# Kernel optimization log

Hardware: AMD Instinct MI355X
Metric: run time of the kernel (lower is better)

The kernel has to match this reference:

```python
import jax, jax.numpy as jnp
import numpy as np

N = 768
SINGLE_DIM = 384
PAIR_DIM = 128
D = 16      # proj_dim per head
H = 12      # n_heads
P = 4       # n_query_points
PV = 8      # n_point_values


def _random_rotations(key, n):
    a = jax.random.normal(key, (n, 3, 3), dtype=jnp.float32)
    q, r = jnp.linalg.qr(a)
    d = jnp.sign(jnp.diagonal(r, axis1=-2, axis2=-1))
    q = q * d[:, None, :]
    det = jnp.linalg.det(q)
    return q * jnp.where(det < 0, -1.0, 1.0)[:, None, None]


def setup_inputs() -> dict:
    key = jax.random.key(0)
    ks = jax.random.split(key, 12)
    s = 0.02
    return {
        "single_rep": jax.random.normal(ks[0], (N, SINGLE_DIM), dtype=jnp.float32),
        "pair_rep": jax.random.normal(ks[1], (N, N, PAIR_DIM), dtype=jnp.float32),
        "rotations": _random_rotations(ks[2], N),
        "translations": jax.random.normal(ks[3], (N, 3), dtype=jnp.float32),
        "Wqkv": s * jax.random.normal(ks[4], (SINGLE_DIM, 3 * H * D), dtype=jnp.float32),
        "Wb": s * jax.random.normal(ks[5], (PAIR_DIM, H), dtype=jnp.float32),
        "Wqk_pts": s * jax.random.normal(ks[6], (SINGLE_DIM, 2 * H * P * 3), dtype=jnp.float32),
        "Wv_pts": s * jax.random.normal(ks[7], (SINGLE_DIM, H * PV * 3), dtype=jnp.float32),
        "gamma": 0.1 * jax.random.normal(ks[8], (H,), dtype=jnp.float32),
        "Wout": s * jax.random.normal(ks[9], (H * (PAIR_DIM + D + PV * 3 + PV), SINGLE_DIM), dtype=jnp.float32),
        "bout": jnp.zeros((SINGLE_DIM,), dtype=jnp.float32),
    }


def _apply_frames(rot, trans, pts):
    # pts: [N, P, H, 3] -> R @ pt + t per residue (dim 0)
    return jnp.einsum('nba,npha->nphb', rot, pts) + trans[:, None, None, :]


def _apply_frames_inv(rot, trans, pts):
    # R^T (pt - t)
    return jnp.einsum('nab,npha->nphb', rot, pts - trans[:, None, None, :])


def reference(single_rep, pair_rep, rotations, translations,
              Wqkv, Wb, Wqk_pts, Wv_pts, gamma, Wout, bout):
    n = single_rep.shape[0]
    sqrt_inv_dim = 1.0 / np.sqrt(D).astype(np.float32)
    w_C = np.sqrt(2.0 / (9.0 * P)).astype(np.float32)
    w_L = np.sqrt(1.0 / 3.0).astype(np.float32)

    qkv = single_rep @ Wqkv                       # [N, 3*H*D]
    q, k, v = jnp.split(qkv, 3, axis=-1)
    q = q.reshape(n, D, H)
    k = k.reshape(n, D, H)
    v = v.reshape(n, D, H)

    b = pair_rep @ Wb                             # [N, N, H]

    qk_pts = single_rep @ Wqk_pts
    q_pts, k_pts = jnp.split(qk_pts, 2, axis=-1)
    q_pts = jnp.moveaxis(q_pts.reshape(n, P, 3, H), -1, -2)   # [N, P, H, 3]
    k_pts = jnp.moveaxis(k_pts.reshape(n, P, 3, H), -1, -2)
    v_pts = jnp.moveaxis((single_rep @ Wv_pts).reshape(n, PV, 3, H), -1, -2)  # [N, PV, H, 3]

    qg = _apply_frames(rotations, translations, q_pts)  # [N, P, H, 3]
    kg = _apply_frames(rotations, translations, k_pts)

    # sum_{p,t} ||qg_i - kg_j||^2 via expansion (avoids [N,N,P,H,3])
    q_sq = jnp.sum(qg * qg, axis=(1, 3))                # [N, H]
    k_sq = jnp.sum(kg * kg, axis=(1, 3))                # [N, H]
    cross = jnp.einsum('ipht,jpht->ijh', qg, kg)        # [N, N, H]
    dist_logits = q_sq[:, None, :] + k_sq[None, :, :] - 2.0 * cross

    dp_logits = sqrt_inv_dim * jnp.einsum('idh,jdh->ijh', q, k) + b
    scale = gamma * (w_C / 2.0)                          # [H]
    a = jax.nn.softmax(w_L * (dp_logits - scale * dist_logits), axis=1)  # [N, N, H]

    out_pair = jnp.einsum('ijh,ijz->izh', a, pair_rep)   # [N, pair_dim, H]
    out_value = jnp.einsum('ijh,jdh->idh', a, v)          # [N, D, H]

    vg = _apply_frames(rotations, translations, v_pts)    # [N, PV, H, 3]
    op = jnp.einsum('ijh,jpht->ipht', a, vg)              # [N, PV, H, 3]
    out_points = _apply_frames_inv(rotations, translations, op)
    out_points_norm = jnp.linalg.norm(out_points, axis=-1)  # [N, PV, H]

    out = jnp.concatenate([
        out_pair.reshape(n, -1),
        out_value.reshape(n, -1),
        out_points.reshape(n, -1),
        out_points_norm.reshape(n, -1),
    ], axis=1)
    return out @ Wout + bout
```

## Files before the change

### kernel.cpp

```cpp
#include <hip/hip_runtime.h>
#include <math.h>

#define NN 768
#define SD 384
#define HH 12

#define W_L 0.57735026918962576f
#define W_C 0.23570226039551584f

typedef __attribute__((ext_vector_type(8))) short short8;
typedef __attribute__((ext_vector_type(4))) short short4_t;
typedef __attribute__((ext_vector_type(4))) float floatx4;
typedef unsigned short ushort_t;
typedef unsigned int uint_t;

__device__ __forceinline__ float wave_max(float v){ for(int o=32;o;o>>=1) v=fmaxf(v,__shfl_xor(v,o)); return v; }
__device__ __forceinline__ float wave_sum(float v){ for(int o=32;o;o>>=1) v+=__shfl_xor(v,o); return v; }

static __device__ __forceinline__ ushort_t f2bf(float f) {
  union { float f; uint_t u; } v; v.f = f;
  uint_t r = (v.u + 0x7FFFu + ((v.u >> 16) & 1u)) >> 16;
  return (ushort_t)r;
}
static __device__ __forceinline__ uint_t pack2bf(float lo, float hi) {
  return ((uint_t)f2bf(hi) << 16) | (uint_t)f2bf(lo);
}

__global__ __launch_bounds__(256) void k1a_gemm(
    const float* __restrict__ single, const float* __restrict__ Wqkv,
    const float* __restrict__ Wqk, const float* __restrict__ Wvp,
    float* __restrict__ raw)
{
  __shared__ float Al[64][17];
  __shared__ float Bl[16][68];
  const int tid = threadIdx.x;
  const int bm = blockIdx.x / 18, bn = blockIdx.x % 18;
  const int tr = tid >> 4, tc = tid & 15;

  const int bcol = bn*64 + (tid & 15)*4;
  const float* Wsrc; int wstride;
  if (bcol < 576)      { Wsrc = Wqkv + bcol;        wstride = 576; }
  else if (bcol < 864) { Wsrc = Wqk  + (bcol-576);  wstride = 288; }
  else                 { Wsrc = Wvp  + (bcol-864);  wstride = 288; }
  const int brow = tid >> 4;
  const int ar = tid >> 2, ac = (tid & 3)*4;

  float4 acc0 = {0,0,0,0}, acc1 = {0,0,0,0}, acc2 = {0,0,0,0}, acc3 = {0,0,0,0};

  for (int kc = 0; kc < 24; ++kc) {
    __syncthreads();
    *(float4*)&Al[ar][ac] = *(const float4*)(single + (size_t)(bm*64+ar)*SD + kc*16 + ac);
    *(float4*)&Bl[brow][(tid&15)*4] = *(const float4*)(Wsrc + (size_t)(kc*16+brow)*wstride);
    __syncthreads();
    #pragma unroll
    for (int kk = 0; kk < 16; ++kk) {
      float a0 = Al[tr*4+0][kk], a1 = Al[tr*4+1][kk], a2 = Al[tr*4+2][kk], a3 = Al[tr*4+3][kk];
      float4 bv = *(float4*)&Bl[kk][tc*4];
      acc0.x += a0*bv.x; acc0.y += a0*bv.y; acc0.z += a0*bv.z; acc0.w += a0*bv.w;
      acc1.x += a1*bv.x; acc1.y += a1*bv.y; acc1.z += a1*bv.z; acc1.w += a1*bv.w;
      acc2.x += a2*bv.x; acc2.y += a2*bv.y; acc2.z += a2*bv.z; acc2.w += a2*bv.w;
      acc3.x += a3*bv.x; acc3.y += a3*bv.y; acc3.z += a3*bv.z; acc3.w += a3*bv.w;
    }
  }
  float* o = raw + (size_t)(bm*64 + tr*4)*1152 + bn*64 + tc*4;
  *(float4*)(o)            = acc0;
  *(float4*)(o + 1152)     = acc1;
  *(float4*)(o + 2*1152)   = acc2;
  *(float4*)(o + 3*1152)   = acc3;
}

__global__ __launch_bounds__(256) void k1b_pack(
    const float* __restrict__ raw_g, const float* __restrict__ rot,
    const float* __restrict__ trans, const float* __restrict__ gamma,
    float* __restrict__ Qt, ushort_t* __restrict__ Ktb, ushort_t* __restrict__ vvT)
{
  __shared__ float raw[4][1152];
  __shared__ float gbuf[4][16][HH][3];
  const int tid = threadIdx.x;
  const int i0 = blockIdx.x * 4;

  for (int s = tid; s < 4*288; s += 256) {
    int r = s / 288, q = s % 288;
    *(float4*)(&raw[r][q*4]) = *(const float4*)(raw_g + (size_t)(i0+r)*1152 + q*4);
  }
  __syncthreads();

  for (int s = tid; s < 4*576; s += 256) {
    int r = s / 576, cc = s % 576;
    int d = (cc % 192) / HH, h = cc % HH;
    int i = i0 + r;
    float val = raw[r][cc];
    if (cc < 192)       Qt[(size_t)i*384 + h*32 + d] = 0.25f*W_L*val;
    else if (cc < 384)  Ktb[(size_t)i*384 + h*32 + d] = f2bf(val);
    else                vvT[(size_t)(h*40 + d)*768 + i] = f2bf(val);
  }
  for (int s = tid; s < 768; s += 256) {
    int r = s / 192, rem = s % 192;
    int slot = rem / HH, h = rem % HH;
    int i = i0 + r;
    int base;
    if (slot < 4) base = 576 + slot*36;
    else if (slot < 8) base = 720 + (slot-4)*36;
    else base = 864 + (slot-8)*36;
    float x0 = raw[r][base + 0*12 + h];
    float x1 = raw[r][base + 1*12 + h];
    float x2 = raw[r][base + 2*12 + h];
    const float* R = rot + (size_t)i*9;
    const float* T = trans + (size_t)i*3;
    float g0 = R[0]*x0 + R[1]*x1 + R[2]*x2 + T[0];
    float g1 = R[3]*x0 + R[4]*x1 + R[5]*x2 + T[1];
    float g2 = R[6]*x0 + R[7]*x1 + R[8]*x2 + T[2];
    gbuf[r][slot][h][0]=g0; gbuf[r][slot][h][1]=g1; gbuf[r][slot][h][2]=g2;
    if (slot < 4) {
      float sc2 = 2.0f*W_L*(gamma[h]*W_C*0.5f);
      float* q = Qt + (size_t)i*384 + h*32 + 16 + slot*3;
      q[0]=sc2*g0; q[1]=sc2*g1; q[2]=sc2*g2;
    } else if (slot < 8) {
      ushort_t* k = Ktb + (size_t)i*384 + h*32 + 16 + (slot-4)*3;
      k[0]=f2bf(g0); k[1]=f2bf(g1); k[2]=f2bf(g2);
    } else {
      ushort_t* vp = vvT + (size_t)(h*40 + 16 + (slot-8)*3)*768 + i;
      vp[0]=f2bf(g0); vp[768]=f2bf(g1); vp[2*768]=f2bf(g2);
    }
  }
  __syncthreads();
  for (int s = tid; s < 96; s += 256) {
    int r = s / 24, rem = s % 24;
    int h = rem / 2, qk = rem % 2;
    int i = i0 + r;
    float sum = 0;
    int b0 = qk ? 4 : 0;
    for (int p = 0; p < 4; ++p)
      for (int t = 0; t < 3; ++t) { float g = gbuf[r][b0+p][h][t]; sum += g*g; }
    float sc = gamma[h]*W_C*0.5f;
    if (qk == 0) {
      float* q = Qt + (size_t)i*384 + h*32;
      q[28] = -W_L*sc; q[29] = -W_L*sc*sum; q[30] = 0.f; q[31] = 0.f;
    } else {
      ushort_t* k = Ktb + (size_t)i*384 + h*32;
      k[28] = f2bf(sum); k[29] = f2bf(1.f); k[30] = 0; k[31] = 0;
    }
  }
}

__global__ __launch_bounds__(256) void k2p_logits(
    const float* __restrict__ pair, const float* __restrict__ Wb,
    const float* __restrict__ Qt, const ushort_t* __restrict__ Ktb,
    float* __restrict__ L)
{
  __shared__ ushort_t Tj[2][64*136];
  __shared__ ushort_t WbT[16*136];
  __shared__ float Qrow[384];
  const int tid = threadIdx.x;
  const int i = blockIdx.x;
  const int lane = tid & 63;
  const int w = tid >> 6;
  const int co = lane & 15, gg = lane >> 4;
  const int srow = tid >> 5, szq = tid & 31;

  for (int s = tid; s < 1536; s += 256) {
    int z = s / 12, h = s % 12;
    WbT[h*136 + z] = f2bf(W_L * Wb[s]);
  }
  for (int s = tid; s < 544; s += 256) WbT[1632 + s] = 0;
  for (int s = tid; s < 384; s += 256) Qrow[s] = Qt[(size_t)i*384 + s];

  const float* src = pair + (size_t)i*NN*128;
  float4 pr[8];
  #pragma unroll
  for (int k = 0; k < 8; ++k)
    pr[k] = *(const float4*)(src + (size_t)(srow + k*8)*128 + szq*4);

  __syncthreads();

  short8 z8, myQ, wb[4];
  #pragma unroll
  for (int s = 0; s < 8; ++s) z8[s] = 0;
  #pragma unroll
  for (int s = 0; s < 8; ++s)
    myQ[s] = (co < 12) ? (short)f2bf(Qrow[co*32 + gg*8 + s]) : (short)0;
  #pragma unroll
  for (int kt = 0; kt < 4; ++kt)
    wb[kt] = *(const short8*)&WbT[co*136 + kt*32 + gg*8];

  const int jb = w*16;

  #pragma unroll 1
  for (int t = 0; t < 12; ++t) {
    const int buf = t & 1;
    #pragma unroll
    for (int k = 0; k < 8; ++k) {
      uint2 uu;
      uu.x = pack2bf(pr[k].x, pr[k].y);
      uu.y = pack2bf(pr[k].z, pr[k].w);
      *(uint2*)&Tj[buf][(srow + k*8)*136 + szq*4] = uu;
    }
    if (t < 11) {
      const float* sn = src + (size_t)(t+1)*64*128;
      #pragma unroll
      for (int k = 0; k < 8; ++k)
        pr[k] = *(const float4*)(sn + (size_t)(srow + k*8)*128 + szq*4);
    }
    __syncthreads();

    floatx4 D; D[0]=0.f; D[1]=0.f; D[2]=0.f; D[3]=0.f;
    #pragma unroll
    for (int kt = 0; kt < 4; ++kt) {
      short8 a = *(const short8*)&Tj[buf][(jb+co)*136 + kt*32 + gg*8];
      D = __builtin_amdgcn_mfma_f32_16x16x32_bf16(a, wb[kt], D, 0, 0, 0);
    }
    const ushort_t* kr = Ktb + (size_t)(t*64 + jb + co)*384;
    #pragma unroll
    for (int kt = 0; kt < 12; ++kt) {
      short8 a = *(const short8*)(kr + kt*32 + gg*8);
      short8 b = (co == kt) ? myQ : z8;
      D = __builtin_amdgcn_mfma_f32_16x16x32_bf16(a, b, D, 0, 0, 0);
    }
    if (co < 12) {
      float4 st = {D[0], D[1], D[2], D[3]};
      *(float4*)(L + ((size_t)i*12 + co)*768 + t*64 + jb + gg*4) = st;
    }
    __syncthreads();
  }
}

__global__ __launch_bounds__(512) void k3_fused(
    const float* __restrict__ pair, const float* __restrict__ L,
    const ushort_t* __restrict__ vvT, const float* __restrict__ rot,
    const float* __restrict__ trans, float* __restrict__ C2)
{
  __shared__ ushort_t PTb[24*512];
  __shared__ ushort_t Tz[2][2][128*20];
  __shared__ float oacc[480];
  const int tid = threadIdx.x;
  const int i = (NN - 1) - blockIdx.x;
  const int w = tid >> 6, lane = tid & 63;
  const int co = lane & 15, gg = lane >> 4;

  const float* psrc = pair + (size_t)i*NN*128;
  const int f0 = tid,       pj0 = f0 >> 5, pz0 = f0 & 31;
  const int f1 = tid + 512, pj1 = f1 >> 5, pz1 = f1 & 31;

  float4 pa0, pa1, pb0, pb1;
  pa0 = *(const float4*)(psrc + (size_t)pj0*128 + pz0*4);
  pa1 = *(const float4*)(psrc + (size_t)pj1*128 + pz1*4);
  pb0 = *(const float4*)(psrc + (size_t)(32 + pj0)*128 + pz0*4);
  pb1 = *(const float4*)(psrc + (size_t)(32 + pj1)*128 + pz1*4);

  const float* Lr = L + (size_t)i*12*768;
  #pragma unroll
  for (int m = 0; m < 2; ++m) {
    if (m == 1 && w >= 4) break;
    const int h = (m == 0) ? w : 8 + w;
    const float* row = Lr + (size_t)h*768;
    float mx = -1e30f;
    #pragma unroll
    for (int k = 0; k < 12; ++k) mx = fmaxf(mx, row[lane + 64*k]);
    mx = wave_max(mx);
    float ev[12]; float sm = 0.f;
    #pragma unroll
    for (int k = 0; k < 12; ++k) { ev[k] = __expf(row[lane + 64*k] - mx); sm += ev[k]; }
    sm = wave_sum(sm);
    const float inv = 1.0f / sm;
    #pragma unroll
    for (int k = 0; k < 12; ++k) {
      int jj = lane + 64*k;
      PTb[(jj >> 5)*512 + h*32 + (jj & 31)] = f2bf(ev[k]*inv);
    }
  }
  for (int s = tid; s < 3072; s += 512) {
    int t = s >> 7, rest = s & 127;
    PTb[t*512 + 384 + rest] = 0;
  }

  floatx4 accZ; accZ[0]=0.f; accZ[1]=0.f; accZ[2]=0.f; accZ[3]=0.f;
  floatx4 accV[4];
  #pragma unroll
  for (int u = 0; u < 4; ++u) { accV[u][0]=0.f; accV[u][1]=0.f; accV[u][2]=0.f; accV[u][3]=0.f; }

  const int sw = (w & 3) << 2;
  const int jb = (gg & 1) * 8;
  const ushort_t* vb0 = vvT + (size_t)((w*4+0)*16 + co)*768 + gg*8;
  const ushort_t* vb1 = vvT + (size_t)((w*4+1)*16 + co)*768 + gg*8;
  const ushort_t* vb2 = vvT + (size_t)((w*4+2)*16 + co)*768 + gg*8;
  const ushort_t* vb3 = vvT + (size_t)((w*4+3)*16 + co)*768 + gg*8;

  auto ITER = [&](int t, float4& r0, float4& r1) {
    const int buf = t & 1;
    {
      const float* p0 = (const float*)&r0;
      const float* p1 = (const float*)&r1;
      ushort_t* tz0 = &Tz[buf][pj0 >> 4][0];
      ushort_t* tz1 = &Tz[buf][pj1 >> 4][0];
      const int jl0 = pj0 & 15, jl1 = pj1 & 15;
      #pragma unroll
      for (int e = 0; e < 4; ++e) {
        int z0 = pz0*4 + e;
        tz0[z0*20 + (jl0 ^ (((z0 >> 4) & 3) << 2))] = f2bf(p0[e]);
        int z1 = pz1*4 + e;
        tz1[z1*20 + (jl1 ^ (((z1 >> 4) & 3) << 2))] = f2bf(p1[e]);
      }
    }
    if (t < 22) {
      const float* sn = psrc + (size_t)(t+2)*32*128;
      r0 = *(const float4*)(sn + (size_t)pj0*128 + pz0*4);
      r1 = *(const float4*)(sn + (size_t)pj1*128 + pz1*4);
    }
    __syncthreads();

    const short8 aP = *(const short8*)&PTb[t*512 + co*32 + gg*8];
    {
      const ushort_t* tz = &Tz[buf][gg >> 1][0];
      const int zrow = (w*16 + co)*20;
      short4_t lo = *(const short4_t*)&tz[zrow + (jb ^ sw)];
      short4_t hi = *(const short4_t*)&tz[zrow + ((jb + 4) ^ sw)];
      short8 bT;
      #pragma unroll
      for (int e = 0; e < 4; ++e) { bT[e] = lo[e]; bT[e+4] = hi[e]; }
      accZ = __builtin_amdgcn_mfma_f32_16x16x32_bf16(aP, bT, accZ, 0, 0, 0);
    }
    {
      const int toff = t*32;
      short8 bV;
      bV = *(const short8*)(vb0 + toff);
      accV[0] = __builtin_amdgcn_mfma_f32_16x16x32_bf16(aP, bV, accV[0], 0, 0, 0);
      bV = *(const short8*)(vb1 + toff);
      accV[1] = __builtin_amdgcn_mfma_f32_16x16x32_bf16(aP, bV, accV[1], 0, 0, 0);
      if (w*4 + 2 < 30) {
        bV = *(const short8*)(vb2 + toff);
        accV[2] = __builtin_amdgcn_mfma_f32_16x16x32_bf16(aP, bV, accV[2], 0, 0, 0);
        bV = *(const short8*)(vb3 + toff);
        accV[3] = __builtin_amdgcn_mfma_f32_16x16x32_bf16(aP, bV, accV[3], 0, 0, 0);
      }
    }
    __syncthreads();
  };

  #pragma unroll 1
  for (int tt = 0; tt < 24; tt += 2) {
    ITER(tt,     pa0, pa1);
    ITER(tt + 1, pb0, pb1);
  }

  float* o = C2 + (size_t)i*2112;
  #pragma unroll
  for (int r = 0; r < 4; ++r) {
    int h = gg*4 + r;
    if (h < 12) o[(w*16 + co)*12 + h] = accZ[r];
  }
  #pragma unroll
  for (int u = 0; u < 4; ++u) {
    int cb = w*4 + u;
    if (cb < 30) {
      int c = cb*16 + co;
      int hc = c / 40;
      #pragma unroll
      for (int r = 0; r < 4; ++r)
        if (gg*4 + r == hc) oacc[c] = accV[u][r];
    }
  }
  __syncthreads();

  if (tid < 96) {
    const int pp = tid / 12, hh = tid % 12;
    const float* R = rot + (size_t)i*9;
    const float* T = trans + (size_t)i*3;
    float x0 = oacc[hh*40+16+pp*3+0] - T[0];
    float x1 = oacc[hh*40+16+pp*3+1] - T[1];
    float x2 = oacc[hh*40+16+pp*3+2] - T[2];
    float y0 = R[0]*x0 + R[3]*x1 + R[6]*x2;
    float y1 = R[1]*x0 + R[4]*x1 + R[7]*x2;
    float y2 = R[2]*x0 + R[5]*x1 + R[8]*x2;
    o[1728 + pp*36 + hh*3 + 0] = y0;
    o[1728 + pp*36 + hh*3 + 1] = y1;
    o[1728 + pp*36 + hh*3 + 2] = y2;
    o[2016 + pp*12 + hh] = sqrtf(y0*y0 + y1*y1 + y2*y2);
  } else if (tid < 288) {
    const int c = tid - 96;
    int d = c / 12, hh = c % 12;
    o[1536 + d*12 + hh] = oacc[hh*40 + d];
  }
}

__global__ __launch_bounds__(256) void k5_out(
    const float* __restrict__ C2, const float* __restrict__ Wout,
    const float* __restrict__ bout, float* __restrict__ out)
{
  __shared__ float Al[32*68];
  __shared__ float Bl[64*36];
  const int tid = threadIdx.x;
  const int bm = blockIdx.x / 12, bn = blockIdx.x % 12;
  const int tr = tid / 16, tc = tid % 16;
  float acc00=0, acc01=0, acc10=0, acc11=0;
  for (int kc = 0; kc < 33; ++kc) {
    __syncthreads();
    for (int s = tid; s < 512; s += 256) {
      int row = s / 16, kq = s % 16;
      *(float4*)(&Al[row*68 + kq*4]) =
        *(const float4*)(C2 + (size_t)(bm*32+row)*2112 + kc*64 + kq*4);
    }
    for (int s = tid; s < 512; s += 256) {
      int kk = s / 8, cq = s % 8;
      *(float4*)(&Bl[kk*36 + cq*4]) =
        *(const float4*)(Wout + (size_t)(kc*64+kk)*384 + bn*32 + cq*4);
    }
    __syncthreads();
    for (int kk = 0; kk < 64; ++kk) {
      float a0 = Al[(tr*2)*68 + kk], a1 = Al[(tr*2+1)*68 + kk];
      float b0 = Bl[kk*36 + tc*2], b1 = Bl[kk*36 + tc*2 + 1];
      acc00 += a0*b0; acc01 += a0*b1;
      acc10 += a1*b0; acc11 += a1*b1;
    }
  }
  int r0 = bm*32 + tr*2, c0 = bn*32 + tc*2;
  out[(size_t)r0*384 + c0]       = acc00 + bout[c0];
  out[(size_t)r0*384 + c0+1]     = acc01 + bout[c0+1];
  out[(size_t)(r0+1)*384 + c0]   = acc10 + bout[c0];
  out[(size_t)(r0+1)*384 + c0+1] = acc11 + bout[c0+1];
}

extern "C" void kernel_launch(void* const* d_in, const int* in_sizes, int n_in,
                              void* d_out, int out_size, void* d_ws, size_t ws_size,
                              hipStream_t stream)
{
  const float* single = (const float*)d_in[0];
  const float* pair   = (const float*)d_in[1];
  const float* rot    = (const float*)d_in[2];
  const float* trans  = (const float*)d_in[3];
  const float* Wqkv   = (const float*)d_in[4];
  const float* Wb     = (const float*)d_in[5];
  const float* Wqk    = (const float*)d_in[6];
  const float* Wvp    = (const float*)d_in[7];
  const float* gamma  = (const float*)d_in[8];
  const float* Wout   = (const float*)d_in[9];
  const float* bout   = (const float*)d_in[10];

  float* ws   = (float*)d_ws;
  float* raw  = ws;
  float* Qt   = raw + (size_t)768*1152;
  float* C2   = Qt  + (size_t)768*384;
  float* L    = C2  + (size_t)768*2112;
  ushort_t* Ktb = (ushort_t*)(L + (size_t)768*12*768);
  ushort_t* vvT = Ktb + (size_t)768*384;
  float* out  = (float*)d_out;

  k1a_gemm<<<dim3(216), dim3(256), 0, stream>>>(single, Wqkv, Wqk, Wvp, raw);
  k1b_pack<<<dim3(192), dim3(256), 0, stream>>>(raw, rot, trans, gamma, Qt, Ktb, vvT);
  k2p_logits<<<dim3(768), dim3(256), 0, stream>>>(pair, Wb, Qt, Ktb, L);
  k3_fused<<<dim3(768), dim3(512), 0, stream>>>(pair, L, vvT, rot, trans, C2);
  k5_out<<<dim3(288), dim3(256), 0, stream>>>(C2, Wout, bout, out);
}
```

Before: 338.2 us.

## Split logits kernel into per-64-column blocks instead of a per-row loop

The logits kernel now launches one block per (row, 64-column tile), 9216 blocks in total, instead of one block per row looping over 12 tiles with a double-buffered register prefetch. Each block loads its K fragments into registers up front, stages one tile of pair data to LDS with a padded stride, and runs the MFMAs once. The goal is more parallelism and better latency hiding across many small blocks, at the price of redoing the Wb/Q setup in every block. A small edit in k3_fused also rewrites the output-store indexing so 96 threads each write two elements.

```diff
diff --git a/kernel.cpp b/kernel.cpp
--- a/kernel.cpp
+++ b/kernel.cpp
@@ -143,20 +143,22 @@
   }
 }
 
-__global__ __launch_bounds__(256) void k2p_logits(
+#define TJS 140
+__global__ __launch_bounds__(256, 3) void k2a_logits(
     const float* __restrict__ pair, const float* __restrict__ Wb,
     const float* __restrict__ Qt, const ushort_t* __restrict__ Ktb,
     float* __restrict__ L)
 {
-  __shared__ ushort_t Tj[2][64*136];
+  __shared__ ushort_t Tj[64*TJS];
   __shared__ ushort_t WbT[16*136];
   __shared__ float Qrow[384];
   const int tid = threadIdx.x;
-  const int i = blockIdx.x;
+  const int i = blockIdx.x / 12;
+  const int j0 = (blockIdx.x % 12) * 64;
   const int lane = tid & 63;
   const int w = tid >> 6;
   const int co = lane & 15, gg = lane >> 4;
-  const int srow = tid >> 5, szq = tid & 31;
+  const int jb = w*16;
 
   for (int s = tid; s < 1536; s += 256) {
     int z = s / 12, h = s % 12;
@@ -165,12 +167,30 @@
   for (int s = tid; s < 544; s += 256) WbT[1632 + s] = 0;
   for (int s = tid; s < 384; s += 256) Qrow[s] = Qt[(size_t)i*384 + s];
 
-  const float* src = pair + (size_t)i*NN*128;
-  float4 pr[8];
-  #pragma unroll
-  for (int k = 0; k < 8; ++k)
-    pr[k] = *(const float4*)(src + (size_t)(srow + k*8)*128 + szq*4);
-
+  short8 kf[12];
+  {
+    const ushort_t* kr = Ktb + (size_t)(j0 + jb + co)*384;
+    #pragma unroll
+    for (int kt = 0; kt < 12; ++kt)
+      kf[kt] = *(const short8*)(kr + kt*32 + gg*8);
+  }
+
+  const float* src = pair + ((size_t)i*NN + j0)*128;
+  float4 pv[8];
+  #pragma unroll
+  for (int k = 0; k < 8; ++k) {
+    int f = tid + k*256;
+    int row = f >> 5, zq = f & 31;
+    pv[k] = *(const float4*)(src + (size_t)row*128 + zq*4);
+  }
+  #pragma unroll
+  for (int k = 0; k < 8; ++k) {
+    int f = tid + k*256;
+    int row = f >> 5, zq = f & 31;
+    uint_t* d = (uint_t*)&Tj[row*TJS + zq*4];
+    d[0] = pack2bf(pv[k].x, pv[k].y);
+    d[1] = pack2bf(pv[k].z, pv[k].w);
+  }
   __syncthreads();
 
   short8 z8, myQ, wb[4];
@@ -183,44 +203,20 @@
   for (int kt = 0; kt < 4; ++kt)
     wb[kt] = *(const short8*)&WbT[co*136 + kt*32 + gg*8];
 
-  const int jb = w*16;
-
-  #pragma unroll 1
-  for (int t = 0; t < 12; ++t) {
-    const int buf = t & 1;
-    #pragma unroll
-    for (int k = 0; k < 8; ++k) {
-      uint2 uu;
-      uu.x = pack2bf(pr[k].x, pr[k].y);
-      uu.y = pack2bf(pr[k].z, pr[k].w);
-      *(uint2*)&Tj[buf][(srow + k*8)*136 + szq*4] = uu;
-    }
-    if (t < 11) {
-      const float* sn = src + (size_t)(t+1)*64*128;
-      #pragma unroll
-      for (int k = 0; k < 8; ++k)
-        pr[k] = *(const float4*)(sn + (size_t)(srow + k*8)*128 + szq*4);
-    }
-    __syncthreads();
-
-    floatx4 D; D[0]=0.f; D[1]=0.f; D[2]=0.f; D[3]=0.f;
-    #pragma unroll
-    for (int kt = 0; kt < 4; ++kt) {
-      short8 a = *(const short8*)&Tj[buf][(jb+co)*136 + kt*32 + gg*8];
-      D = __builtin_amdgcn_mfma_f32_16x16x32_bf16(a, wb[kt], D, 0, 0, 0);
-    }
-    const ushort_t* kr = Ktb + (size_t)(t*64 + jb + co)*384;
-    #pragma unroll
-    for (int kt = 0; kt < 12; ++kt) {
-      short8 a = *(const short8*)(kr + kt*32 + gg*8);
-      short8 b = (co == kt) ? myQ : z8;
-      D = __builtin_amdgcn_mfma_f32_16x16x32_bf16(a, b, D, 0, 0, 0);
-    }
-    if (co < 12) {
-      float4 st = {D[0], D[1], D[2], D[3]};
-      *(float4*)(L + ((size_t)i*12 + co)*768 + t*64 + jb + gg*4) = st;
-    }
-    __syncthreads();
+  floatx4 D; D[0]=0.f; D[1]=0.f; D[2]=0.f; D[3]=0.f;
+  #pragma unroll
+  for (int kt = 0; kt < 4; ++kt) {
+    short8 a = *(const short8*)&Tj[(jb+co)*TJS + kt*32 + gg*8];
+    D = __builtin_amdgcn_mfma_f32_16x16x32_bf16(a, wb[kt], D, 0, 0, 0);
+  }
+  #pragma unroll
+  for (int kt = 0; kt < 12; ++kt) {
+    short8 b = (co == kt) ? myQ : z8;
+    D = __builtin_amdgcn_mfma_f32_16x16x32_bf16(kf[kt], b, D, 0, 0, 0);
+  }
+  if (co < 12) {
+    float4 st = {D[0], D[1], D[2], D[3]};
+    *(float4*)(L + ((size_t)i*12 + co)*768 + j0 + jb + gg*4) = st;
   }
 }
 
@@ -375,10 +371,11 @@
     o[1728 + pp*36 + hh*3 + 1] = y1;
     o[1728 + pp*36 + hh*3 + 2] = y2;
     o[2016 + pp*12 + hh] = sqrtf(y0*y0 + y1*y1 + y2*y2);
-  } else if (tid < 288) {
+  } else if (tid < 192) {
     const int c = tid - 96;
-    int d = c / 12, hh = c % 12;
-    o[1536 + d*12 + hh] = oacc[hh*40 + d];
+    float* ob = C2 + (size_t)i*2112 + 1536;
+    ob[c]      = oacc[(c%12)*40 + (c/12)];
+    ob[c+96]   = oacc[((c+96)%12)*40 + ((c+96)/12)];
   }
 }
 
@@ -446,7 +443,7 @@
 
   k1a_gemm<<<dim3(216), dim3(256), 0, stream>>>(single, Wqkv, Wqk, Wvp, raw);
   k1b_pack<<<dim3(192), dim3(256), 0, stream>>>(raw, rot, trans, gamma, Qt, Ktb, vvT);
-  k2p_logits<<<dim3(768), dim3(256), 0, stream>>>(pair, Wb, Qt, Ktb, L);
+  k2a_logits<<<dim3(9216), dim3(256), 0, stream>>>(pair, Wb, Qt, Ktb, L);
   k3_fused<<<dim3(768), dim3(512), 0, stream>>>(pair, L, vvT, rot, trans, C2);
   k5_out<<<dim3(288), dim3(256), 0, stream>>>(C2, Wout, bout, out);
 }
```

Result: faster. 321.3 us (-5.0%).
